# Optimization experiments

Measured on AMD Instinct MI355X. Metric: run time of the kernel, lower is better.

The kernel has to match this reference:

```python
import jax, jax.numpy as jnp
import numpy as np


def setup_inputs() -> dict:
    key = jax.random.key(0)
    k1, k2, k3 = jax.random.split(key, 3)
    B, T1, T2, D = 16, 1024, 1024, 256
    x = jax.random.normal(k1, (B, T1, D), dtype=jnp.float32)
    y = jax.random.normal(k2, (B, T2, D), dtype=jnp.float32)
    WS = jax.random.normal(k3, (3 * D,), dtype=jnp.float32) * 0.05
    return {"x": x, "y": y, "WS": WS}


def reference(x, y, WS):
    # BiDAF trilinear similarity. Original computes
    #   S[b,i,j] = sum_k concat([x_i, 1, x_i])_k * concat([1, y_j, y_j])_k * WS_k
    # which decomposes exactly into:
    #   S = x @ w1 (broadcast over j) + y @ w2 (broadcast over i) + (x * w3) @ y^T
    D = x.shape[-1]
    w1, w2, w3 = WS[:D], WS[D:2 * D], WS[2 * D:]
    term_x = jnp.einsum('bid,d->bi', x, w1)            # [B, T1]
    term_y = jnp.einsum('bjd,d->bj', y, w2)            # [B, T2]
    term_xy = jnp.einsum('bid,bjd->bij', x * w3, y)    # [B, T1, T2]
    return term_xy + term_x[:, :, None] + term_y[:, None, :]
```

## Files before the change

### kernel.cpp

```cpp
#include <hip/hip_runtime.h>

#define DK 256
#define TT 1024
#define NB 16

typedef __attribute__((ext_vector_type(8))) short bf16x8;
typedef __attribute__((ext_vector_type(8))) unsigned short u16x8;
typedef __attribute__((ext_vector_type(4))) float f32x4;

__device__ __forceinline__ unsigned short f2bf(float f) {
    unsigned int u = __float_as_uint(f);
    unsigned int r = 0x7fffu + ((u >> 16) & 1u);
    return (unsigned short)((u + r) >> 16);
}

__global__ __launch_bounds__(512, 4) void fused_kernel(
    const float* __restrict__ x, const float* __restrict__ y,
    const float* __restrict__ WS, float* __restrict__ out)
{
    __shared__ unsigned short Bs[128 * DK];
    __shared__ float tys[128];

    const int tid  = threadIdx.x;
    const int lane = tid & 63;
    const int w    = tid >> 6;

    const int id = blockIdx.x;
    const int b  = id & 15;
    const int is = (id >> 4) & 3;
    const int jt = id >> 6;

    {
        const float* gY0 = y + ((size_t)b * TT + jt * 128) * DK;
        #pragma unroll
        for (int it = 0; it < 8; ++it) {
            const int g = it * 512 + tid;
            const int j = g >> 5;
            const int c = g & 31;
            const float* gY  = gY0 + (size_t)j * DK + c * 8;
            const float* w3p = WS + 2 * DK + c * 8;
            const float* w2p = WS + DK + c * 8;
            const float4 ya = *(const float4*)(gY);
            const float4 yb = *(const float4*)(gY + 4);
            const float4 wa = *(const float4*)(w3p);
            const float4 wb = *(const float4*)(w3p + 4);
            const float4 va = *(const float4*)(w2p);
            const float4 vb = *(const float4*)(w2p + 4);
            float p = ya.x * va.x + ya.y * va.y + ya.z * va.z + ya.w * va.w
                    + yb.x * vb.x + yb.y * vb.y + yb.z * vb.z + yb.w * vb.w;
            u16x8 o;
            o[0] = f2bf(ya.x * wa.x); o[1] = f2bf(ya.y * wa.y);
            o[2] = f2bf(ya.z * wa.z); o[3] = f2bf(ya.w * wa.w);
            o[4] = f2bf(yb.x * wb.x); o[5] = f2bf(yb.y * wb.y);
            o[6] = f2bf(yb.z * wb.z); o[7] = f2bf(yb.w * wb.w);
            const int slot = c ^ (j & 7);
            *(u16x8*)(Bs + j * DK + slot * 8) = o;
            p += __shfl_xor(p, 1);
            p += __shfl_xor(p, 2);
            p += __shfl_xor(p, 4);
            p += __shfl_xor(p, 8);
            p += __shfl_xor(p, 16);
            if ((tid & 31) == 0) tys[j] = p;
        }
    }
    __syncthreads();

    const int mfr  = lane & 15;
    const int quad = lane >> 4;
    const int i0   = is * 256 + w * 32;
    const float* gA = x + ((size_t)b * TT + i0) * DK;

    f32x4 acc[2][8];
    #pragma unroll
    for (int it = 0; it < 2; ++it)
        #pragma unroll
        for (int n = 0; n < 8; ++n)
            acc[it][n] = (f32x4){0.f, 0.f, 0.f, 0.f};
    float txp[2] = {0.f, 0.f};

    #pragma unroll
    for (int ks = 0; ks < 8; ++ks) {
        const float* w1p = WS + ks * 32 + quad * 8;
        const float4 w1a = *(const float4*)(w1p);
        const float4 w1b = *(const float4*)(w1p + 4);
        bf16x8 av[2];
        #pragma unroll
        for (int it = 0; it < 2; ++it) {
            const float* rp = gA + (size_t)(it * 16 + mfr) * DK
                              + ks * 32 + quad * 8;
            const float4 xa = *(const float4*)rp;
            const float4 xb = *(const float4*)(rp + 4);
            txp[it] += xa.x * w1a.x + xa.y * w1a.y + xa.z * w1a.z + xa.w * w1a.w
                     + xb.x * w1b.x + xb.y * w1b.y + xb.z * w1b.z + xb.w * w1b.w;
            bf16x8 a;
            a[0] = (short)f2bf(xa.x); a[1] = (short)f2bf(xa.y);
            a[2] = (short)f2bf(xa.z); a[3] = (short)f2bf(xa.w);
            a[4] = (short)f2bf(xb.x); a[5] = (short)f2bf(xb.y);
            a[6] = (short)f2bf(xb.z); a[7] = (short)f2bf(xb.w);
            av[it] = a;
        }
        #pragma unroll
        for (int n = 0; n < 8; ++n) {
            const int j    = n * 16 + mfr;
            const int slot = (ks * 4 + quad) ^ (j & 7);
            const bf16x8 bv = *(const bf16x8*)(Bs + j * DK + slot * 8);
            #pragma unroll
            for (int it = 0; it < 2; ++it)
                acc[it][n] = __builtin_amdgcn_mfma_f32_16x16x32_bf16(
                    av[it], bv, acc[it][n], 0, 0, 0);
        }
    }

    #pragma unroll
    for (int it = 0; it < 2; ++it) {
        txp[it] += __shfl_xor(txp[it], 16);
        txp[it] += __shfl_xor(txp[it], 32);
    }

    float tyv[8];
    #pragma unroll
    for (int n = 0; n < 8; ++n)
        tyv[n] = tys[n * 16 + mfr];

    float* outB = out + ((size_t)b << 20) + (size_t)i0 * TT + jt * 128;
    #pragma unroll
    for (int it = 0; it < 2; ++it) {
        #pragma unroll
        for (int r = 0; r < 4; ++r) {
            const int row = it * 16 + quad * 4 + r;
            const float trow = __shfl(txp[it], (lane & 48) | (quad * 4 + r));
            #pragma unroll
            for (int n = 0; n < 8; ++n)
                outB[(size_t)row * TT + n * 16 + mfr] =
                    acc[it][n][r] + trow + tyv[n];
        }
    }
}

extern "C" void kernel_launch(void* const* d_in, const int* in_sizes, int n_in,
                              void* d_out, int out_size, void* d_ws, size_t ws_size,
                              hipStream_t stream)
{
    const float* x  = (const float*)d_in[0];
    const float* y  = (const float*)d_in[1];
    const float* WS = (const float*)d_in[2];
    float* out = (float*)d_out;
    (void)d_ws; (void)ws_size;

    fused_kernel<<<dim3(512), dim3(512), 0, stream>>>(x, y, WS, out);
}
```

Before: 109.6 us.

## Halve tiles and split K staging to raise occupancy; nontemporal output stores

Each block now covers 128 rows instead of 256, so there are twice as many blocks (1024). The Y operand is staged through LDS in two K-halves of 128, which halves shared memory per block, and launch bounds are raised to 6 blocks per CU. The bf16 conversion now packs pairs into 32-bit words, output writes use nontemporal stores, and the block index order changes so neighbouring blocks share the same Y tile. The cost is an extra barrier per block, and because Y is staged twice as often in total, Y reads and the w3 scaling work double.

```diff
diff --git a/kernel.cpp b/kernel.cpp
--- a/kernel.cpp
+++ b/kernel.cpp
@@ -5,7 +5,6 @@
 #define NB 16
 
 typedef __attribute__((ext_vector_type(8))) short bf16x8;
-typedef __attribute__((ext_vector_type(8))) unsigned short u16x8;
 typedef __attribute__((ext_vector_type(4))) float f32x4;
 
 __device__ __forceinline__ unsigned short f2bf(float f) {
@@ -13,12 +12,21 @@
     unsigned int r = 0x7fffu + ((u >> 16) & 1u);
     return (unsigned short)((u + r) >> 16);
 }
+__device__ __forceinline__ unsigned int pack2(float a, float b) {
+    return (unsigned int)f2bf(a) | ((unsigned int)f2bf(b) << 16);
+}
+__device__ __forceinline__ bf16x8 cvt8(const float4 a, const float4 b) {
+    union { unsigned int u[4]; bf16x8 v; } r;
+    r.u[0] = pack2(a.x, a.y); r.u[1] = pack2(a.z, a.w);
+    r.u[2] = pack2(b.x, b.y); r.u[3] = pack2(b.z, b.w);
+    return r.v;
+}
 
-__global__ __launch_bounds__(512, 4) void fused_kernel(
+__global__ __launch_bounds__(512, 6) void fused_kernel(
     const float* __restrict__ x, const float* __restrict__ y,
     const float* __restrict__ WS, float* __restrict__ out)
 {
-    __shared__ unsigned short Bs[128 * DK];
+    __shared__ unsigned short Bs[128 * 128];
     __shared__ float tys[128];
 
     const int tid  = threadIdx.x;
@@ -26,114 +34,100 @@
     const int w    = tid >> 6;
 
     const int id = blockIdx.x;
-    const int b  = id & 15;
-    const int is = (id >> 4) & 3;
-    const int jt = id >> 6;
+    const int jt = id >> 7;
+    const int b  = (id >> 3) & 15;
+    const int is = id & 7;
 
-    {
-        const float* gY0 = y + ((size_t)b * TT + jt * 128) * DK;
+    const int mfr  = lane & 15;
+    const int quad = lane >> 4;
+
+    const float* gY0 = y + ((size_t)b * TT + jt * 128) * DK;
+    const float* gA0 = x + ((size_t)b * TT + is * 128 + w * 16 + mfr) * DK;
+
+    const int sj = tid >> 4;
+    const int sc = tid & 15;
+
+    f32x4 acc[8];
+    #pragma unroll
+    for (int n = 0; n < 8; ++n)
+        acc[n] = (f32x4){0.f, 0.f, 0.f, 0.f};
+    float txp = 0.f;
+
+    #pragma unroll
+    for (int kh = 0; kh < 2; ++kh) {
+        if (kh) __syncthreads();
+
         #pragma unroll
-        for (int it = 0; it < 8; ++it) {
-            const int g = it * 512 + tid;
-            const int j = g >> 5;
-            const int c = g & 31;
-            const float* gY  = gY0 + (size_t)j * DK + c * 8;
-            const float* w3p = WS + 2 * DK + c * 8;
-            const float* w2p = WS + DK + c * 8;
-            const float4 ya = *(const float4*)(gY);
-            const float4 yb = *(const float4*)(gY + 4);
+        for (int q = 0; q < 4; ++q) {
+            const int j = q * 32 + sj;
+            const float* src = gY0 + (size_t)j * DK + kh * 128 + sc * 8;
+            const float* w3p = WS + 2 * DK + kh * 128 + sc * 8;
+            const float* w2p = WS + DK + kh * 128 + sc * 8;
+            const float4 ya = *(const float4*)(src);
+            const float4 yb = *(const float4*)(src + 4);
             const float4 wa = *(const float4*)(w3p);
             const float4 wb = *(const float4*)(w3p + 4);
             const float4 va = *(const float4*)(w2p);
             const float4 vb = *(const float4*)(w2p + 4);
             float p = ya.x * va.x + ya.y * va.y + ya.z * va.z + ya.w * va.w
                     + yb.x * vb.x + yb.y * vb.y + yb.z * vb.z + yb.w * vb.w;
-            u16x8 o;
-            o[0] = f2bf(ya.x * wa.x); o[1] = f2bf(ya.y * wa.y);
-            o[2] = f2bf(ya.z * wa.z); o[3] = f2bf(ya.w * wa.w);
-            o[4] = f2bf(yb.x * wb.x); o[5] = f2bf(yb.y * wb.y);
-            o[6] = f2bf(yb.z * wb.z); o[7] = f2bf(yb.w * wb.w);
-            const int slot = c ^ (j & 7);
-            *(u16x8*)(Bs + j * DK + slot * 8) = o;
+            const float4 pa = make_float4(ya.x * wa.x, ya.y * wa.y,
+                                          ya.z * wa.z, ya.w * wa.w);
+            const float4 pb = make_float4(yb.x * wb.x, yb.y * wb.y,
+                                          yb.z * wb.z, yb.w * wb.w);
+            const bf16x8 o = cvt8(pa, pb);
+            const int slot = sc ^ (j & 7);
+            *(bf16x8*)(Bs + j * 128 + slot * 8) = o;
             p += __shfl_xor(p, 1);
             p += __shfl_xor(p, 2);
             p += __shfl_xor(p, 4);
             p += __shfl_xor(p, 8);
-            p += __shfl_xor(p, 16);
-            if ((tid & 31) == 0) tys[j] = p;
+            if (sc == 0) {
+                if (kh) tys[j] += p; else tys[j] = p;
+            }
         }
-    }
-    __syncthreads();
+        __syncthreads();
 
-    const int mfr  = lane & 15;
-    const int quad = lane >> 4;
-    const int i0   = is * 256 + w * 32;
-    const float* gA = x + ((size_t)b * TT + i0) * DK;
-
-    f32x4 acc[2][8];
-    #pragma unroll
-    for (int it = 0; it < 2; ++it)
         #pragma unroll
-        for (int n = 0; n < 8; ++n)
-            acc[it][n] = (f32x4){0.f, 0.f, 0.f, 0.f};
-    float txp[2] = {0.f, 0.f};
-
-    #pragma unroll
-    for (int ks = 0; ks < 8; ++ks) {
-        const float* w1p = WS + ks * 32 + quad * 8;
-        const float4 w1a = *(const float4*)(w1p);
-        const float4 w1b = *(const float4*)(w1p + 4);
-        bf16x8 av[2];
-        #pragma unroll
-        for (int it = 0; it < 2; ++it) {
-            const float* rp = gA + (size_t)(it * 16 + mfr) * DK
-                              + ks * 32 + quad * 8;
-            const float4 xa = *(const float4*)rp;
-            const float4 xb = *(const float4*)(rp + 4);
-            txp[it] += xa.x * w1a.x + xa.y * w1a.y + xa.z * w1a.z + xa.w * w1a.w
-                     + xb.x * w1b.x + xb.y * w1b.y + xb.z * w1b.z + xb.w * w1b.w;
-            bf16x8 a;
-            a[0] = (short)f2bf(xa.x); a[1] = (short)f2bf(xa.y);
-            a[2] = (short)f2bf(xa.z); a[3] = (short)f2bf(xa.w);
-            a[4] = (short)f2bf(xb.x); a[5] = (short)f2bf(xb.y);
-            a[6] = (short)f2bf(xb.z); a[7] = (short)f2bf(xb.w);
-            av[it] = a;
-        }
-        #pragma unroll
-        for (int n = 0; n < 8; ++n) {
-            const int j    = n * 16 + mfr;
-            const int slot = (ks * 4 + quad) ^ (j & 7);
-            const bf16x8 bv = *(const bf16x8*)(Bs + j * DK + slot * 8);
+        for (int ks = 0; ks < 4; ++ks) {
+            const int k0 = kh * 128 + ks * 32 + quad * 8;
+            const float4 xa = *(const float4*)(gA0 + k0);
+            const float4 xb = *(const float4*)(gA0 + k0 + 4);
+            const float4 w1a = *(const float4*)(WS + k0);
+            const float4 w1b = *(const float4*)(WS + k0 + 4);
+            txp += xa.x * w1a.x + xa.y * w1a.y + xa.z * w1a.z + xa.w * w1a.w
+                 + xb.x * w1b.x + xb.y * w1b.y + xb.z * w1b.z + xb.w * w1b.w;
+            const bf16x8 av = cvt8(xa, xb);
             #pragma unroll
-            for (int it = 0; it < 2; ++it)
-                acc[it][n] = __builtin_amdgcn_mfma_f32_16x16x32_bf16(
-                    av[it], bv, acc[it][n], 0, 0, 0);
+            for (int n = 0; n < 8; ++n) {
+                const int j    = n * 16 + mfr;
+                const int slot = (ks * 4 + quad) ^ (j & 7);
+                const bf16x8 bv = *(const bf16x8*)(Bs + j * 128 + slot * 8);
+                acc[n] = __builtin_amdgcn_mfma_f32_16x16x32_bf16(
+                    av, bv, acc[n], 0, 0, 0);
+            }
         }
     }
 
-    #pragma unroll
-    for (int it = 0; it < 2; ++it) {
-        txp[it] += __shfl_xor(txp[it], 16);
-        txp[it] += __shfl_xor(txp[it], 32);
-    }
+    txp += __shfl_xor(txp, 16);
+    txp += __shfl_xor(txp, 32);
 
     float tyv[8];
     #pragma unroll
     for (int n = 0; n < 8; ++n)
         tyv[n] = tys[n * 16 + mfr];
 
-    float* outB = out + ((size_t)b << 20) + (size_t)i0 * TT + jt * 128;
+    float* outB = out + ((size_t)b << 20)
+                + (size_t)(is * 128 + w * 16) * TT + jt * 128;
     #pragma unroll
-    for (int it = 0; it < 2; ++it) {
+    for (int r = 0; r < 4; ++r) {
+        const int row = quad * 4 + r;
+        const float trow = __shfl(txp, (lane & 48) | row);
         #pragma unroll
-        for (int r = 0; r < 4; ++r) {
-            const int row = it * 16 + quad * 4 + r;
-            const float trow = __shfl(txp[it], (lane & 48) | (quad * 4 + r));
-            #pragma unroll
-            for (int n = 0; n < 8; ++n)
-                outB[(size_t)row * TT + n * 16 + mfr] =
-                    acc[it][n][r] + trow + tyv[n];
-        }
+        for (int n = 0; n < 8; ++n)
+            __builtin_nontemporal_store(
+                acc[n][r] + trow + tyv[n],
+                &outB[(size_t)row * TT + n * 16 + mfr]);
     }
 }
 
@@ -147,5 +141,5 @@
     float* out = (float*)d_out;
     (void)d_ws; (void)ws_size;
 
-    fused_kernel<<<dim3(512), dim3(512), 0, stream>>>(x, y, WS, out);
+    fused_kernel<<<dim3(1024), dim3(512), 0, stream>>>(x, y, WS, out);
 }
```

After: 196.1 us. 1.79x slower.
